# Optimization experiments

Measured on AMD Instinct MI355X. Metric: run time of the kernel, lower is better.

The kernel has to match this reference:

```python
import jax, jax.numpy as jnp
import numpy as np

HIDDEN = 896
NUM_Q_HEADS = 14
NUM_KV_HEADS = 2
HEAD_DIM = 64
ROPE_BASE = 10000.0
B, S = 4, 2048


def rotate_half(x):
    x1, x2 = jnp.split(x, 2, axis=-1)
    return jnp.concatenate((-x2, x1), axis=-1)


def rope_cos_sin(position_ids):
    # position_ids: [B, S] int -> cos/sin [B, 1, S, HEAD_DIM]
    inv_freq = 1.0 / (ROPE_BASE ** (jnp.arange(0, HEAD_DIM, 2, dtype=jnp.float32) / HEAD_DIM))
    freqs = position_ids.astype(jnp.float32)[..., None] * inv_freq  # [B,S,D/2]
    emb = jnp.concatenate((freqs, freqs), axis=-1)  # [B,S,D]
    return jnp.cos(emb)[:, None, :, :], jnp.sin(emb)[:, None, :, :]


def setup_inputs() -> dict:
    key = jax.random.key(0)
    k1, k2, k3, k4, k5 = jax.random.split(key, 5)
    s = 1.0 / np.sqrt(HIDDEN)
    return {
        "hidden_states": jax.random.normal(k1, (B, S, HIDDEN), dtype=jnp.float32),
        "position_ids": jnp.broadcast_to(jnp.arange(S, dtype=jnp.int64), (B, S)),
        "Wq": jax.random.normal(k2, (HIDDEN, NUM_Q_HEADS * HEAD_DIM), dtype=jnp.float32) * s,
        "Wk": jax.random.normal(k3, (HIDDEN, NUM_KV_HEADS * HEAD_DIM), dtype=jnp.float32) * s,
        "Wv": jax.random.normal(k4, (HIDDEN, NUM_KV_HEADS * HEAD_DIM), dtype=jnp.float32) * s,
        "Wo": jax.random.normal(k5, (NUM_Q_HEADS * HEAD_DIM, HIDDEN), dtype=jnp.float32) * s,
    }


def reference(hidden_states, position_ids, Wq, Wk, Wv, Wo):
    b, s, _ = hidden_states.shape
    n_rep = NUM_Q_HEADS // NUM_KV_HEADS

    q = (hidden_states @ Wq).reshape(b, s, NUM_Q_HEADS, HEAD_DIM).transpose(0, 2, 1, 3)   # [B,Hq,S,D]
    k = (hidden_states @ Wk).reshape(b, s, NUM_KV_HEADS, HEAD_DIM).transpose(0, 2, 1, 3)  # [B,Hkv,S,D]
    v = (hidden_states @ Wv).reshape(b, s, NUM_KV_HEADS, HEAD_DIM).transpose(0, 2, 1, 3)

    cos, sin = rope_cos_sin(position_ids)  # [B,1,S,D]
    q = q * cos + rotate_half(q) * sin
    k = k * cos + rotate_half(k) * sin

    # repeat_interleave KV heads to match query heads
    k = jnp.repeat(k, n_rep, axis=1)  # [B,Hq,S,D]
    v = jnp.repeat(v, n_rep, axis=1)

    scale = 1.0 / jnp.sqrt(jnp.float32(HEAD_DIM))
    attn = jnp.einsum('bhqd,bhkd->bhqk', q, k) * scale  # [B,Hq,S,S]
    attn = jax.nn.softmax(attn, axis=-1)
    out = jnp.einsum('bhqk,bhkd->bhqd', attn, v)  # [B,Hq,S,D]
    out = out.transpose(0, 2, 1, 3).reshape(b, s, NUM_Q_HEADS * HEAD_DIM)
    return out @ Wo
```

## Files before the change

### kernel.cpp

```cpp
#include <hip/hip_runtime.h>
#include <hip/hip_bf16.h>
#include <math.h>

typedef unsigned short ushort_t;
typedef __bf16 bf16x8 __attribute__((ext_vector_type(8)));
typedef float f32x4 __attribute__((ext_vector_type(4)));

#define HIDDEN 896
#define NQH 14
#define NKVH 2
#define HD 64
#define SEQ 2048
#define NBATCH 4

__device__ inline ushort_t f2bf(float x) {
  union { float f; unsigned u; } c; c.f = x;
  unsigned r = c.u + 0x7FFFu + ((c.u >> 16) & 1u);
  return (ushort_t)(r >> 16);
}

__device__ inline unsigned pack2bf(float a, float b) {
  union { float f; unsigned u; } ca, cb; ca.f = a; cb.f = b;
  unsigned ua = ca.u + 0x8000u, ub = cb.u + 0x8000u;
  return __builtin_amdgcn_perm(ub, ua, 0x07060302);
}

__device__ inline bf16x8 ldfrag(const ushort_t* p) {
  return *reinterpret_cast<const bf16x8*>(p);
}

__device__ inline void async16(const ushort_t* g, ushort_t* l) {
  __builtin_amdgcn_global_load_lds(
      (const __attribute__((address_space(1))) void*)g,
      (__attribute__((address_space(3))) void*)l, 16, 0, 0);
}


__device__ inline void transpose_sec(const float* __restrict__ in, ushort_t* __restrict__ out,
                                     int K, int N, int bx, int by) {
  __shared__ float tile[32][33];
  int k0 = by * 32, n0 = bx * 32;
  for (int r = threadIdx.y; r < 32; r += 8) {
    int k = k0 + r, n = n0 + threadIdx.x;
    tile[r][threadIdx.x] = (k < K && n < N) ? in[(size_t)k * N + n] : 0.f;
  }
  __syncthreads();
  for (int r = threadIdx.y; r < 32; r += 8) {
    int n = n0 + r, k = k0 + threadIdx.x;
    if (n < N && k < K) out[(size_t)n * K + k] = f2bf(tile[threadIdx.x][r]);
  }
}

__global__ void k_prep(const float* __restrict__ hidden, ushort_t* __restrict__ hb,
                       const float* __restrict__ Wq, const float* __restrict__ Wk,
                       const float* __restrict__ Wv, const float* __restrict__ Wo,
                       ushort_t* __restrict__ wT, ushort_t* __restrict__ woT,
                       float2* __restrict__ ctab) {
  const int blk = blockIdx.x;
  const int tid = threadIdx.y * 32 + threadIdx.x;
  if (blk < 7168) {
    int i = blk * 256 + tid;
    float4 v = reinterpret_cast<const float4*>(hidden)[i];
    ushort4 o;
    o.x = f2bf(v.x); o.y = f2bf(v.y); o.z = f2bf(v.z); o.w = f2bf(v.w);
    reinterpret_cast<ushort4*>(hb)[i] = o;
  } else if (blk < 7424) {
    int idx = (blk - 7168) * 256 + tid;
    int s = idx >> 5, dp = idx & 31;
    float inv = exp2f(-(float)dp * 0.41524101186092596f);
    float ang = (float)s * inv;
    float sn, cn;
    sincosf(ang, &sn, &cn);
    ctab[idx] = make_float2(cn, sn);
  } else if (blk < 8208) {
    int t = blk - 7424;
    transpose_sec(Wq, wT, 896, 896, t % 28, t / 28);
  } else if (blk < 8320) {
    int t = blk - 8208;
    transpose_sec(Wk, wT + (size_t)896 * 896, 896, 128, t % 4, t / 4);
  } else if (blk < 8432) {
    int t = blk - 8320;
    transpose_sec(Wv, wT + (size_t)1024 * 896, 896, 128, t % 4, t / 4);
  } else {
    int t = blk - 8432;
    transpose_sec(Wo, woT, 896, 896, t % 28, t / 28);
  }
}

__global__ __launch_bounds__(256) void k_qkv(
    const ushort_t* __restrict__ hb,
    const ushort_t* __restrict__ wT,
    const int* __restrict__ pos_ids,
    const float2* __restrict__ ctab,
    ushort_t* __restrict__ Qg,
    ushort_t* __restrict__ Kg,
    ushort_t* __restrict__ Vtg) {
  __shared__ ushort_t smem[16384];
  ushort_t* sa = smem;
  ushort_t* sbb = smem + 8192;

  const int f = blockIdx.x;
  const int x = f & 7, s8 = f >> 3;
  const int sect = s8 % 9;
  const int mt = (s8 / 9) * 8 + x;
  const int nt0 = sect * 128;
  const int m0 = mt * 128;
  const int tid = threadIdx.x;
  const int wave = tid >> 6, lane = tid & 63;
  const int l15 = lane & 15, quad = lane >> 4;
  const int wm = wave >> 1, wn = wave & 1;
  const int sw = l15 & 7;

  f32x4 acc[4][4];
  const f32x4 z4 = {0.f, 0.f, 0.f, 0.f};
#pragma unroll
  for (int a = 0; a < 4; ++a)
#pragma unroll
    for (int b = 0; b < 4; ++b) acc[a][b] = z4;

  for (int kt = 0; kt < 14; ++kt) {
    const int k0 = kt * 64;
    __syncthreads();
#pragma unroll
    for (int i = 0; i < 4; ++i) {
      int id = i * 256 + tid;
      int row = id >> 3;
      int cs = (id & 7) ^ (row & 7);
      int base = (i * 256 + wave * 64) * 8;
      async16(hb + (size_t)(m0 + row) * HIDDEN + k0 + cs * 8, sa + base);
      async16(wT + (size_t)(nt0 + row) * HIDDEN + k0 + cs * 8, sbb + base);
    }
    __syncthreads();
    bf16x8 af[4][2], bf[4][2];
#pragma unroll
    for (int kc = 0; kc < 2; ++kc) {
      int c = kc * 4 + quad;
#pragma unroll
      for (int mb = 0; mb < 4; ++mb)
        af[mb][kc] = ldfrag(sa + ((wm * 64 + mb * 16 + l15) * 8 + (c ^ sw)) * 8);
#pragma unroll
      for (int nb = 0; nb < 4; ++nb)
        bf[nb][kc] = ldfrag(sbb + ((wn * 64 + nb * 16 + l15) * 8 + (c ^ sw)) * 8);
    }
#pragma unroll
    for (int mb = 0; mb < 4; ++mb)
#pragma unroll
      for (int nb = 0; nb < 4; ++nb) {
        acc[mb][nb] = __builtin_amdgcn_mfma_f32_16x16x32_bf16(af[mb][0], bf[nb][0], acc[mb][nb], 0, 0, 0);
        acc[mb][nb] = __builtin_amdgcn_mfma_f32_16x16x32_bf16(af[mb][1], bf[nb][1], acc[mb][nb], 0, 0, 0);
      }
  }

  if (sect < 8) {
    const bool isQ = sect < 7;
    const float csc = isQ ? 0.125f * 1.4426950408889634f : 1.0f;
    ushort_t* dst = isQ ? Qg : Kg;
    const int nheads = isQ ? NQH : NKVH;
    const int hh = isQ ? sect * 2 + wn : wn;
#pragma unroll
    for (int mb = 0; mb < 4; ++mb)
#pragma unroll
      for (int r = 0; r < 4; ++r) {
        int token = m0 + wm * 64 + mb * 16 + quad * 4 + r;
        int b = token >> 11, s = token & 2047;
        int pos = pos_ids[token];
        size_t base = ((size_t)(b * nheads + hh) * SEQ + s) * HD;
#pragma unroll
        for (int nb = 0; nb < 2; ++nb) {
          float2 cs = ctab[pos * 32 + nb * 16 + l15];
          float x0 = acc[mb][nb][r];
          float x1 = acc[mb][nb + 2][r];
          float y0 = (x0 * cs.x - x1 * cs.y) * csc;
          float y1 = (x1 * cs.x + x0 * cs.y) * csc;
          dst[base + nb * 16 + l15]      = f2bf(y0);
          dst[base + nb * 16 + l15 + 32] = f2bf(y1);
        }
      }
  } else {
    __syncthreads();
    ushort_t* vt = smem;
#pragma unroll
    for (int mb = 0; mb < 4; ++mb) {
      int tl = wm * 64 + mb * 16 + quad * 4;
      int chunk = tl >> 3, ofs = tl & 7;
#pragma unroll
      for (int nb = 0; nb < 4; ++nb) {
        int row = wn * 64 + nb * 16 + l15;
        int slot = chunk ^ (row & 7);
        ushort_t* p = vt + row * 128 + slot * 8 + ofs;
        *reinterpret_cast<unsigned*>(p)     = pack2bf(acc[mb][nb][0], acc[mb][nb][1]);
        *reinterpret_cast<unsigned*>(p + 2) = pack2bf(acc[mb][nb][2], acc[mb][nb][3]);
      }
    }
    __syncthreads();
    const int bb = m0 >> 11, s0 = m0 & 2047;
#pragma unroll
    for (int i = 0; i < 8; ++i) {
      int id = i * 256 + tid;
      int row = id >> 4, ch = id & 15;
      int kvh = row >> 6, d = row & 63;
      int slot = ch ^ (row & 7);
      uint4 v = *reinterpret_cast<const uint4*>(vt + row * 128 + slot * 8);
      *reinterpret_cast<uint4*>(Vtg + ((size_t)(bb * NKVH + kvh) * HD + d) * SEQ + s0 + ch * 8) = v;
    }
  }
}

__global__ __launch_bounds__(64, 2) void k_attn(
    const ushort_t* __restrict__ Qg,
    const ushort_t* __restrict__ Kg,
    const ushort_t* __restrict__ Vtg,
    ushort_t* __restrict__ attn) {
  __shared__ ushort_t pbuf[64 * 72];

  const int f = blockIdx.x;
  const int x = f & 7, s8 = f >> 3;
  const int lh = s8 % 7;
  const int qc = s8 / 7;
  const int b = x >> 1, kvh = x & 1;
  const int h = kvh * 7 + lh;
  const int bh = b * NQH + h;
  const int lane = threadIdx.x;
  const int l15 = lane & 15, quad = lane >> 4;
  const int q0 = qc * 64;

  bf16x8 qf[4][2];
#pragma unroll
  for (int qs = 0; qs < 4; ++qs) {
    const size_t qb = ((size_t)bh * SEQ + q0 + qs * 16 + l15) * HD + quad * 8;
    qf[qs][0] = ldfrag(Qg + qb);
    qf[qs][1] = ldfrag(Qg + qb + 32);
  }

  bf16x8 ones;
#pragma unroll
  for (int i = 0; i < 8; ++i) ones[i] = (__bf16)1.0f;

  const ushort_t* Kb = Kg + (size_t)(b * NKVH + kvh) * SEQ * HD;
  const ushort_t* Vb = Vtg + (size_t)(b * NKVH + kvh) * HD * SEQ;

  f32x4 o[4][4];
  f32x4 lfr[4];
  const f32x4 z4 = {0.f, 0.f, 0.f, 0.f};
#pragma unroll
  for (int qs = 0; qs < 4; ++qs) {
    lfr[qs] = z4;
#pragma unroll
    for (int nb = 0; nb < 4; ++nb) o[qs][nb] = z4;
  }

  for (int jt = 0; jt < 32; ++jt) {
    const int s0 = jt * 64;

#pragma unroll
    for (int nb = 0; nb < 4; ++nb) {
      const ushort_t* kr = Kb + (size_t)(s0 + nb * 16 + l15) * HD + quad * 8;
      bf16x8 kf0 = ldfrag(kr);
      bf16x8 kf1 = ldfrag(kr + 32);
#pragma unroll
      for (int qs = 0; qs < 4; ++qs) {
        f32x4 t = z4;
        t = __builtin_amdgcn_mfma_f32_16x16x32_bf16(kf0, qf[qs][0], t, 0, 0, 0);
        t = __builtin_amdgcn_mfma_f32_16x16x32_bf16(kf1, qf[qs][1], t, 0, 0, 0);
        float p0 = __builtin_amdgcn_exp2f(t[0]);
        float p1 = __builtin_amdgcn_exp2f(t[1]);
        float p2 = __builtin_amdgcn_exp2f(t[2]);
        float p3 = __builtin_amdgcn_exp2f(t[3]);
        uint2 d;
        d.x = pack2bf(p0, p1);
        d.y = pack2bf(p2, p3);
        *reinterpret_cast<uint2*>(pbuf + (qs * 16 + l15) * 72 + nb * 16 + quad * 4) = d;
      }
    }

    bf16x8 pf[4][2];
#pragma unroll
    for (int qs = 0; qs < 4; ++qs) {
      pf[qs][0] = ldfrag(pbuf + (qs * 16 + l15) * 72 + quad * 8);
      pf[qs][1] = ldfrag(pbuf + (qs * 16 + l15) * 72 + 32 + quad * 8);
      lfr[qs] = __builtin_amdgcn_mfma_f32_16x16x32_bf16(pf[qs][0], ones, lfr[qs], 0, 0, 0);
      lfr[qs] = __builtin_amdgcn_mfma_f32_16x16x32_bf16(pf[qs][1], ones, lfr[qs], 0, 0, 0);
    }

#pragma unroll
    for (int nb = 0; nb < 4; ++nb) {
      const ushort_t* vr = Vb + (size_t)(nb * 16 + l15) * SEQ + s0 + quad * 8;
      bf16x8 vf0 = ldfrag(vr);
      bf16x8 vf1 = ldfrag(vr + 32);
#pragma unroll
      for (int qs = 0; qs < 4; ++qs) {
        o[qs][nb] = __builtin_amdgcn_mfma_f32_16x16x32_bf16(pf[qs][0], vf0, o[qs][nb], 0, 0, 0);
        o[qs][nb] = __builtin_amdgcn_mfma_f32_16x16x32_bf16(pf[qs][1], vf1, o[qs][nb], 0, 0, 0);
      }
    }
  }

#pragma unroll
  for (int qs = 0; qs < 4; ++qs) {
#pragma unroll
    for (int r = 0; r < 4; ++r) {
      float inv = __builtin_amdgcn_rcpf(lfr[qs][r]);
      int qg = q0 + qs * 16 + quad * 4 + r;
#pragma unroll
      for (int nb = 0; nb < 4; ++nb) {
        float val = o[qs][nb][r] * inv;
        attn[(size_t)(b * SEQ + qg) * (NQH * HD) + h * HD + nb * 16 + l15] = f2bf(val);
      }
    }
  }
}

__global__ __launch_bounds__(256) void k_oproj(
    const ushort_t* __restrict__ attn,
    const ushort_t* __restrict__ woT,
    float* __restrict__ out) {
  __shared__ ushort_t smem[16384];
  ushort_t* sa = smem;
  ushort_t* sbb = smem + 8192;

  const int f = blockIdx.x;
  const int x = f & 7, s8 = f >> 3;
  const int n_sect = s8 % 7;
  const int mt = (s8 / 7) * 8 + x;
  const int n0 = n_sect * 128;
  const int m0 = mt * 128;
  const int tid = threadIdx.x;
  const int wave = tid >> 6, lane = tid & 63;
  const int l15 = lane & 15, quad = lane >> 4;
  const int wm = wave >> 1, wn = wave & 1;
  const int sw = l15 & 7;

  f32x4 acc[4][4];
  const f32x4 z4 = {0.f, 0.f, 0.f, 0.f};
#pragma unroll
  for (int a = 0; a < 4; ++a)
#pragma unroll
    for (int b = 0; b < 4; ++b) acc[a][b] = z4;

  for (int kt = 0; kt < 14; ++kt) {
    const int k0 = kt * 64;
    __syncthreads();
#pragma unroll
    for (int i = 0; i < 4; ++i) {
      int id = i * 256 + tid;
      int row = id >> 3;
      int cs = (id & 7) ^ (row & 7);
      int base = (i * 256 + wave * 64) * 8;
      async16(attn + (size_t)(m0 + row) * HIDDEN + k0 + cs * 8, sa + base);
      async16(woT + (size_t)(n0 + row) * HIDDEN + k0 + cs * 8, sbb + base);
    }
    __syncthreads();
    bf16x8 af[4][2], bf[4][2];
#pragma unroll
    for (int kc = 0; kc < 2; ++kc) {
      int c = kc * 4 + quad;
#pragma unroll
      for (int mb = 0; mb < 4; ++mb)
        af[mb][kc] = ldfrag(sa + ((wm * 64 + mb * 16 + l15) * 8 + (c ^ sw)) * 8);
#pragma unroll
      for (int nb = 0; nb < 4; ++nb)
        bf[nb][kc] = ldfrag(sbb + ((wn * 64 + nb * 16 + l15) * 8 + (c ^ sw)) * 8);
    }
#pragma unroll
    for (int mb = 0; mb < 4; ++mb)
#pragma unroll
      for (int nb = 0; nb < 4; ++nb) {
        acc[mb][nb] = __builtin_amdgcn_mfma_f32_16x16x32_bf16(af[mb][0], bf[nb][0], acc[mb][nb], 0, 0, 0);
        acc[mb][nb] = __builtin_amdgcn_mfma_f32_16x16x32_bf16(af[mb][1], bf[nb][1], acc[mb][nb], 0, 0, 0);
      }
  }

#pragma unroll
  for (int mb = 0; mb < 4; ++mb)
#pragma unroll
    for (int nb = 0; nb < 4; ++nb)
#pragma unroll
      for (int r = 0; r < 4; ++r)
        out[(size_t)(m0 + wm * 64 + mb * 16 + quad * 4 + r) * HIDDEN +
            n0 + wn * 64 + nb * 16 + l15] = acc[mb][nb][r];
}


extern "C" void kernel_launch(void* const* d_in, const int* in_sizes, int n_in,
                              void* d_out, int out_size, void* d_ws, size_t ws_size,
                              hipStream_t stream) {
  (void)in_sizes; (void)n_in; (void)out_size; (void)ws_size;
  const float* hidden = (const float*)d_in[0];
  const int* pos      = (const int*)d_in[1];
  const float* Wq     = (const float*)d_in[2];
  const float* Wk     = (const float*)d_in[3];
  const float* Wv     = (const float*)d_in[4];
  const float* Wo     = (const float*)d_in[5];
  float* out = (float*)d_out;

  char* ws = (char*)d_ws;
  ushort_t* hb   = (ushort_t*)(ws);
  ushort_t* wT   = (ushort_t*)(ws + 14680064);
  float2*   ctab = (float2*)  (ws + 16744448);
  ushort_t* Qg   = (ushort_t*)(ws + 17268736);
  ushort_t* Kg   = (ushort_t*)(ws + 31948800);
  ushort_t* Vtg  = (ushort_t*)(ws + 34045952);
  ushort_t* attn = (ushort_t*)(ws + 36143104);
  ushort_t* woT  = (ushort_t*)(ws + 50823168);

  k_prep<<<9216, dim3(32, 8), 0, stream>>>(hidden, hb, Wq, Wk, Wv, Wo, wT, woT, ctab);
  k_qkv<<<576, 256, 0, stream>>>(hb, wT, pos, ctab, Qg, Kg, Vtg);
  k_attn<<<1792, 64, 0, stream>>>(Qg, Kg, Vtg, attn);
  k_oproj<<<448, 256, 0, stream>>>(attn, woT, out);
}
```

Measured before the change: 254.9 us.

## Split attention KV loop across two waves and halve GEMM M-tiles

The attention kernel now runs two waves per block. Each wave handles alternating 64-key tiles with its own P buffer, and the partial O and row sums are merged through shared memory before normalising. This doubles the parallelism per query chunk without needing a running max, since the softmax has no max subtraction. The QKV and O-projection GEMMs use 64-row M-tiles instead of 128, doubling the grid size to improve CU occupancy and wave balance, at the cost of less reuse of the B tile.

New measurement: 357.3 us. 40.2% more time.

```diff
diff --git a/kernel.cpp b/kernel.cpp
--- a/kernel.cpp
+++ b/kernel.cpp
@@ -95,55 +95,60 @@
     ushort_t* __restrict__ Qg,
     ushort_t* __restrict__ Kg,
     ushort_t* __restrict__ Vtg) {
-  __shared__ ushort_t smem[16384];
+  __shared__ ushort_t smem[12288];
   ushort_t* sa = smem;
-  ushort_t* sbb = smem + 8192;
+  ushort_t* sbb = smem + 4096;
 
   const int f = blockIdx.x;
   const int x = f & 7, s8 = f >> 3;
   const int sect = s8 % 9;
   const int mt = (s8 / 9) * 8 + x;
   const int nt0 = sect * 128;
-  const int m0 = mt * 128;
+  const int m0 = mt * 64;
   const int tid = threadIdx.x;
   const int wave = tid >> 6, lane = tid & 63;
   const int l15 = lane & 15, quad = lane >> 4;
   const int wm = wave >> 1, wn = wave & 1;
   const int sw = l15 & 7;
 
-  f32x4 acc[4][4];
+  f32x4 acc[2][4];
   const f32x4 z4 = {0.f, 0.f, 0.f, 0.f};
 #pragma unroll
-  for (int a = 0; a < 4; ++a)
+  for (int a = 0; a < 2; ++a)
 #pragma unroll
     for (int b = 0; b < 4; ++b) acc[a][b] = z4;
 
   for (int kt = 0; kt < 14; ++kt) {
     const int k0 = kt * 64;
     __syncthreads();
+#pragma unroll
+    for (int i = 0; i < 2; ++i) {
+      int id = i * 256 + tid;
+      int row = id >> 3;
+      int cs = (id & 7) ^ (row & 7);
+      async16(hb + (size_t)(m0 + row) * HIDDEN + k0 + cs * 8, sa + (i * 256 + wave * 64) * 8);
+    }
 #pragma unroll
     for (int i = 0; i < 4; ++i) {
       int id = i * 256 + tid;
       int row = id >> 3;
       int cs = (id & 7) ^ (row & 7);
-      int base = (i * 256 + wave * 64) * 8;
-      async16(hb + (size_t)(m0 + row) * HIDDEN + k0 + cs * 8, sa + base);
-      async16(wT + (size_t)(nt0 + row) * HIDDEN + k0 + cs * 8, sbb + base);
-    }
-    __syncthreads();
-    bf16x8 af[4][2], bf[4][2];
+      async16(wT + (size_t)(nt0 + row) * HIDDEN + k0 + cs * 8, sbb + (i * 256 + wave * 64) * 8);
+    }
+    __syncthreads();
+    bf16x8 af[2][2], bf[4][2];
 #pragma unroll
     for (int kc = 0; kc < 2; ++kc) {
       int c = kc * 4 + quad;
 #pragma unroll
-      for (int mb = 0; mb < 4; ++mb)
-        af[mb][kc] = ldfrag(sa + ((wm * 64 + mb * 16 + l15) * 8 + (c ^ sw)) * 8);
+      for (int mb = 0; mb < 2; ++mb)
+        af[mb][kc] = ldfrag(sa + ((wm * 32 + mb * 16 + l15) * 8 + (c ^ sw)) * 8);
 #pragma unroll
       for (int nb = 0; nb < 4; ++nb)
         bf[nb][kc] = ldfrag(sbb + ((wn * 64 + nb * 16 + l15) * 8 + (c ^ sw)) * 8);
     }
 #pragma unroll
-    for (int mb = 0; mb < 4; ++mb)
+    for (int mb = 0; mb < 2; ++mb)
 #pragma unroll
       for (int nb = 0; nb < 4; ++nb) {
         acc[mb][nb] = __builtin_amdgcn_mfma_f32_16x16x32_bf16(af[mb][0], bf[nb][0], acc[mb][nb], 0, 0, 0);
@@ -158,10 +163,10 @@
     const int nheads = isQ ? NQH : NKVH;
     const int hh = isQ ? sect * 2 + wn : wn;
 #pragma unroll
-    for (int mb = 0; mb < 4; ++mb)
-#pragma unroll
-      for (int r = 0; r < 4; ++r) {
-        int token = m0 + wm * 64 + mb * 16 + quad * 4 + r;
+    for (int mb = 0; mb < 2; ++mb)
+#pragma unroll
+      for (int r = 0; r < 4; ++r) {
+        int token = m0 + wm * 32 + mb * 16 + quad * 4 + r;
         int b = token >> 11, s = token & 2047;
         int pos = pos_ids[token];
         size_t base = ((size_t)(b * nheads + hh) * SEQ + s) * HD;
@@ -180,14 +185,14 @@
     __syncthreads();
     ushort_t* vt = smem;
 #pragma unroll
-    for (int mb = 0; mb < 4; ++mb) {
-      int tl = wm * 64 + mb * 16 + quad * 4;
+    for (int mb = 0; mb < 2; ++mb) {
+      int tl = wm * 32 + mb * 16 + quad * 4;
       int chunk = tl >> 3, ofs = tl & 7;
 #pragma unroll
       for (int nb = 0; nb < 4; ++nb) {
         int row = wn * 64 + nb * 16 + l15;
         int slot = chunk ^ (row & 7);
-        ushort_t* p = vt + row * 128 + slot * 8 + ofs;
+        ushort_t* p = vt + row * 64 + slot * 8 + ofs;
         *reinterpret_cast<unsigned*>(p)     = pack2bf(acc[mb][nb][0], acc[mb][nb][1]);
         *reinterpret_cast<unsigned*>(p + 2) = pack2bf(acc[mb][nb][2], acc[mb][nb][3]);
       }
@@ -195,23 +200,24 @@
     __syncthreads();
     const int bb = m0 >> 11, s0 = m0 & 2047;
 #pragma unroll
-    for (int i = 0; i < 8; ++i) {
+    for (int i = 0; i < 4; ++i) {
       int id = i * 256 + tid;
-      int row = id >> 4, ch = id & 15;
+      int row = id >> 3, ch = id & 7;
       int kvh = row >> 6, d = row & 63;
       int slot = ch ^ (row & 7);
-      uint4 v = *reinterpret_cast<const uint4*>(vt + row * 128 + slot * 8);
+      uint4 v = *reinterpret_cast<const uint4*>(vt + row * 64 + slot * 8);
       *reinterpret_cast<uint4*>(Vtg + ((size_t)(bb * NKVH + kvh) * HD + d) * SEQ + s0 + ch * 8) = v;
     }
   }
 }
 
-__global__ __launch_bounds__(64, 2) void k_attn(
+__global__ __launch_bounds__(128, 4) void k_attn(
     const ushort_t* __restrict__ Qg,
     const ushort_t* __restrict__ Kg,
     const ushort_t* __restrict__ Vtg,
     ushort_t* __restrict__ attn) {
-  __shared__ ushort_t pbuf[64 * 72];
+  __shared__ ushort_t pbuf[2][64 * 72];
+  __shared__ float lbuf[64];
 
   const int f = blockIdx.x;
   const int x = f & 7, s8 = f >> 3;
@@ -220,9 +226,11 @@
   const int b = x >> 1, kvh = x & 1;
   const int h = kvh * 7 + lh;
   const int bh = b * NQH + h;
-  const int lane = threadIdx.x;
+  const int tid = threadIdx.x;
+  const int wave = tid >> 6, lane = tid & 63;
   const int l15 = lane & 15, quad = lane >> 4;
   const int q0 = qc * 64;
+  ushort_t* pw = pbuf[wave];
 
   bf16x8 qf[4][2];
 #pragma unroll
@@ -249,8 +257,8 @@
     for (int nb = 0; nb < 4; ++nb) o[qs][nb] = z4;
   }
 
-  for (int jt = 0; jt < 32; ++jt) {
-    const int s0 = jt * 64;
+  for (int jt = 0; jt < 16; ++jt) {
+    const int s0 = (jt * 2 + wave) * 64;
 
 #pragma unroll
     for (int nb = 0; nb < 4; ++nb) {
@@ -269,15 +277,15 @@
         uint2 d;
         d.x = pack2bf(p0, p1);
         d.y = pack2bf(p2, p3);
-        *reinterpret_cast<uint2*>(pbuf + (qs * 16 + l15) * 72 + nb * 16 + quad * 4) = d;
+        *reinterpret_cast<uint2*>(pw + (qs * 16 + l15) * 72 + nb * 16 + quad * 4) = d;
       }
     }
 
     bf16x8 pf[4][2];
 #pragma unroll
     for (int qs = 0; qs < 4; ++qs) {
-      pf[qs][0] = ldfrag(pbuf + (qs * 16 + l15) * 72 + quad * 8);
-      pf[qs][1] = ldfrag(pbuf + (qs * 16 + l15) * 72 + 32 + quad * 8);
+      pf[qs][0] = ldfrag(pw + (qs * 16 + l15) * 72 + quad * 8);
+      pf[qs][1] = ldfrag(pw + (qs * 16 + l15) * 72 + 32 + quad * 8);
       lfr[qs] = __builtin_amdgcn_mfma_f32_16x16x32_bf16(pf[qs][0], ones, lfr[qs], 0, 0, 0);
       lfr[qs] = __builtin_amdgcn_mfma_f32_16x16x32_bf16(pf[qs][1], ones, lfr[qs], 0, 0, 0);
     }
@@ -295,18 +303,63 @@
     }
   }
 
-#pragma unroll
-  for (int qs = 0; qs < 4; ++qs) {
-#pragma unroll
-    for (int r = 0; r < 4; ++r) {
-      float inv = __builtin_amdgcn_rcpf(lfr[qs][r]);
-      int qg = q0 + qs * 16 + quad * 4 + r;
-#pragma unroll
-      for (int nb = 0; nb < 4; ++nb) {
-        float val = o[qs][nb][r] * inv;
-        attn[(size_t)(b * SEQ + qg) * (NQH * HD) + h * HD + nb * 16 + l15] = f2bf(val);
-      }
-    }
+  float* fb = reinterpret_cast<float*>(pbuf[1]);
+  if (wave == 1) {
+#pragma unroll
+    for (int qs = 0; qs < 4; ++qs)
+#pragma unroll
+      for (int r = 0; r < 4; ++r) {
+        int q = qs * 16 + quad * 4 + r;
+        fb[q * 33 + l15]      = o[qs][0][r];
+        fb[q * 33 + 16 + l15] = o[qs][1][r];
+        if (l15 == 0) lbuf[q] = lfr[qs][r];
+      }
+  }
+  __syncthreads();
+  if (wave == 0) {
+#pragma unroll
+    for (int qs = 0; qs < 4; ++qs)
+#pragma unroll
+      for (int r = 0; r < 4; ++r) {
+        int q = qs * 16 + quad * 4 + r;
+        o[qs][0][r] += fb[q * 33 + l15];
+        o[qs][1][r] += fb[q * 33 + 16 + l15];
+        lfr[qs][r] += lbuf[q];
+      }
+  }
+  __syncthreads();
+  if (wave == 1) {
+#pragma unroll
+    for (int qs = 0; qs < 4; ++qs)
+#pragma unroll
+      for (int r = 0; r < 4; ++r) {
+        int q = qs * 16 + quad * 4 + r;
+        fb[q * 33 + l15]      = o[qs][2][r];
+        fb[q * 33 + 16 + l15] = o[qs][3][r];
+      }
+  }
+  __syncthreads();
+  if (wave == 0) {
+#pragma unroll
+    for (int qs = 0; qs < 4; ++qs)
+#pragma unroll
+      for (int r = 0; r < 4; ++r) {
+        int q = qs * 16 + quad * 4 + r;
+        o[qs][2][r] += fb[q * 33 + l15];
+        o[qs][3][r] += fb[q * 33 + 16 + l15];
+      }
+#pragma unroll
+    for (int qs = 0; qs < 4; ++qs)
+#pragma unroll
+      for (int r = 0; r < 4; ++r) {
+        float inv = 1.0f / lfr[qs][r];
+        int qg = q0 + qs * 16 + quad * 4 + r;
+#pragma unroll
+        for (int nb = 0; nb < 4; ++nb) {
+          float val = o[qs][nb][r] * inv;
+          attn[(size_t)(b * SEQ + qg) * (NQH * HD) + h * HD + nb * 16 + l15] = f2bf(val);
+        }
+      }
   }
 }
 
@@ -314,55 +367,60 @@
     const ushort_t* __restrict__ attn,
     const ushort_t* __restrict__ woT,
     float* __restrict__ out) {
-  __shared__ ushort_t smem[16384];
+  __shared__ ushort_t smem[12288];
   ushort_t* sa = smem;
-  ushort_t* sbb = smem + 8192;
+  ushort_t* sbb = smem + 4096;
 
   const int f = blockIdx.x;
   const int x = f & 7, s8 = f >> 3;
   const int n_sect = s8 % 7;
   const int mt = (s8 / 7) * 8 + x;
   const int n0 = n_sect * 128;
-  const int m0 = mt * 128;
+  const int m0 = mt * 64;
   const int tid = threadIdx.x;
   const int wave = tid >> 6, lane = tid & 63;
   const int l15 = lane & 15, quad = lane >> 4;
   const int wm = wave >> 1, wn = wave & 1;
   const int sw = l15 & 7;
 
-  f32x4 acc[4][4];
+  f32x4 acc[2][4];
   const f32x4 z4 = {0.f, 0.f, 0.f, 0.f};
 #pragma unroll
-  for (int a = 0; a < 4; ++a)
+  for (int a = 0; a < 2; ++a)
 #pragma unroll
     for (int b = 0; b < 4; ++b) acc[a][b] = z4;
 
   for (int kt = 0; kt < 14; ++kt) {
     const int k0 = kt * 64;
     __syncthreads();
+#pragma unroll
+    for (int i = 0; i < 2; ++i) {
+      int id = i * 256 + tid;
+      int row = id >> 3;
+      int cs = (id & 7) ^ (row & 7);
+      async16(attn + (size_t)(m0 + row) * HIDDEN + k0 + cs * 8, sa + (i * 256 + wave * 64) * 8);
+    }
 #pragma unroll
     for (int i = 0; i < 4; ++i) {
       int id = i * 256 + tid;
       int row = id >> 3;
       int cs = (id & 7) ^ (row & 7);
-      int base = (i * 256 + wave * 64) * 8;
-      async16(attn + (size_t)(m0 + row) * HIDDEN + k0 + cs * 8, sa + base);
-      async16(woT + (size_t)(n0 + row) * HIDDEN + k0 + cs * 8, sbb + base);
-    }
-    __syncthreads();
-    bf16x8 af[4][2], bf[4][2];
+      async16(woT + (size_t)(n0 + row) * HIDDEN + k0 + cs * 8, sbb + (i * 256 + wave * 64) * 8);
+    }
+    __syncthreads();
+    bf16x8 af[2][2], bf[4][2];
 #pragma unroll
     for (int kc = 0; kc < 2; ++kc) {
       int c = kc * 4 + quad;
 #pragma unroll
-      for (int mb = 0; mb < 4; ++mb)
-        af[mb][kc] = ldfrag(sa + ((wm * 64 + mb * 16 + l15) * 8 + (c ^ sw)) * 8);
+      for (int mb = 0; mb < 2; ++mb)
+        af[mb][kc] = ldfrag(sa + ((wm * 32 + mb * 16 + l15) * 8 + (c ^ sw)) * 8);
 #pragma unroll
       for (int nb = 0; nb < 4; ++nb)
         bf[nb][kc] = ldfrag(sbb + ((wn * 64 + nb * 16 + l15) * 8 + (c ^ sw)) * 8);
     }
 #pragma unroll
-    for (int mb = 0; mb < 4; ++mb)
+    for (int mb = 0; mb < 2; ++mb)
 #pragma unroll
       for (int nb = 0; nb < 4; ++nb) {
         acc[mb][nb] = __builtin_amdgcn_mfma_f32_16x16x32_bf16(af[mb][0], bf[nb][0], acc[mb][nb], 0, 0, 0);
@@ -371,12 +429,12 @@
   }
 
 #pragma unroll
-  for (int mb = 0; mb < 4; ++mb)
+  for (int mb = 0; mb < 2; ++mb)
 #pragma unroll
     for (int nb = 0; nb < 4; ++nb)
 #pragma unroll
       for (int r = 0; r < 4; ++r)
-        out[(size_t)(m0 + wm * 64 + mb * 16 + quad * 4 + r) * HIDDEN +
+        out[(size_t)(m0 + wm * 32 + mb * 16 + quad * 4 + r) * HIDDEN +
             n0 + wn * 64 + nb * 16 + l15] = acc[mb][nb][r];
 }
 
@@ -404,7 +462,7 @@
   ushort_t* woT  = (ushort_t*)(ws + 50823168);
 
   k_prep<<<9216, dim3(32, 8), 0, stream>>>(hidden, hb, Wq, Wk, Wv, Wo, wT, woT, ctab);
-  k_qkv<<<576, 256, 0, stream>>>(hb, wT, pos, ctab, Qg, Kg, Vtg);
-  k_attn<<<1792, 64, 0, stream>>>(Qg, Kg, Vtg, attn);
-  k_oproj<<<448, 256, 0, stream>>>(attn, woT, out);
-}
+  k_qkv<<<1152, 256, 0, stream>>>(hb, wT, pos, ctab, Qg, Kg, Vtg);
+  k_attn<<<1792, 128, 0, stream>>>(Qg, Kg, Vtg, attn);
+  k_oproj<<<896, 256, 0, stream>>>(attn, woT, out);
+}
```
